# Kernel tuning notes

Hardware: AMD Instinct MI355X
Metric: run time of the kernel (lower is better)

## Reference

```python
import jax, jax.numpy as jnp
import numpy as np

NUM_HEADS = 16
D_MODEL = 1024
D_K = D_MODEL // NUM_HEADS
THETA = 10000.0
SEQ_LEN = 2048
BATCH = 2


def _rope(x, token_positions):
    # x: [B, H, S, d_k]; token_positions: [S] int
    d_k = x.shape[-1]
    inv_freq = THETA ** (-jnp.arange(0, d_k, 2, dtype=jnp.float32) / d_k)  # [d_k/2]
    ang = token_positions.astype(jnp.float32)[:, None] * inv_freq[None, :]  # [S, d_k/2]
    cos, sin = jnp.cos(ang), jnp.sin(ang)
    x_even = x[..., ::2]
    x_odd = x[..., 1::2]
    rot_even = x_even * cos - x_odd * sin
    rot_odd = x_even * sin + x_odd * cos
    return jnp.stack([rot_even, rot_odd], axis=-1).reshape(x.shape)


def setup_inputs() -> dict:
    key = jax.random.key(0)
    kx, kq, kk, kv, ko = jax.random.split(key, 5)
    sigma = float(np.sqrt(2.0 / (D_MODEL + D_MODEL)))
    x = jax.random.normal(kx, (BATCH, SEQ_LEN, D_MODEL), dtype=jnp.float32)
    Wq = jax.random.truncated_normal(kq, -3.0, 3.0, (D_MODEL, D_MODEL), jnp.float32) * sigma
    Wk = jax.random.truncated_normal(kk, -3.0, 3.0, (D_MODEL, D_MODEL), jnp.float32) * sigma
    Wv = jax.random.truncated_normal(kv, -3.0, 3.0, (D_MODEL, D_MODEL), jnp.float32) * sigma
    Wo = jax.random.truncated_normal(ko, -3.0, 3.0, (D_MODEL, D_MODEL), jnp.float32) * sigma
    token_positions = jnp.arange(SEQ_LEN, dtype=jnp.int32)
    return {"x": x, "Wq": Wq, "Wk": Wk, "Wv": Wv, "Wo": Wo, "token_positions": token_positions}


def reference(x, Wq, Wk, Wv, Wo, token_positions):
    bs, seq_len, _ = x.shape
    # Linear stores W as [out, in]: out = einsum('...i,oi->...o')
    def proj(W):
        h = jnp.einsum('bsi,oi->bso', x, W)
        return h.reshape(bs, seq_len, NUM_HEADS, D_K).transpose(0, 2, 1, 3)  # [B,H,S,d_k]
    Q = _rope(proj(Wq), token_positions)
    K = _rope(proj(Wk), token_positions)
    V = proj(Wv)
    scores = jnp.einsum('bhqd,bhkd->bhqk', Q, K) / jnp.sqrt(jnp.float32(D_K))
    causal = jnp.tril(jnp.ones((seq_len, seq_len), dtype=bool))
    scores = jnp.where(causal[None, None], scores, -jnp.inf)
    probs = jax.nn.softmax(scores, axis=-1)
    attn = jnp.einsum('bhqk,bhkd->bhqd', probs, V)
    attn = attn.transpose(0, 2, 1, 3).reshape(bs, seq_len, NUM_HEADS * D_K)
    return jnp.einsum('bsi,oi->bso', attn, Wo)
```

## Files before the change

kernel.cpp:

```cpp
#include <hip/hip_runtime.h>
#include <math.h>

#define SEQ  2048
#define DM   1024
#define NH   16
#define DK   64
#define MTOT 4096
#define BATCH 2

typedef __attribute__((ext_vector_type(8))) short bf16x8;
typedef __attribute__((ext_vector_type(4))) float f32x4;

#define CSC 0.18033688011112042f

__device__ __forceinline__ ushort f2bf(float f) {
    unsigned u = __builtin_bit_cast(unsigned, f);
    u += 0x7FFFu + ((u >> 16) & 1u);
    return (ushort)(u >> 16);
}

__device__ __forceinline__ void async_ld16(const void* g, void* l) {
    __builtin_amdgcn_global_load_lds(
        (const __attribute__((address_space(1))) void*)g,
        (__attribute__((address_space(3))) void*)l, 16, 0, 0);
}


__global__ __launch_bounds__(256) void convert_kernel(
    const float* __restrict__ X, const float* __restrict__ Wq,
    const float* __restrict__ Wk, const float* __restrict__ Wv,
    const float* __restrict__ Wo, const int* __restrict__ pos,
    ushort* __restrict__ Xb, ushort* __restrict__ Wqkvb,
    ushort* __restrict__ Wob, float2* __restrict__ rtab)
{
    const int y = blockIdx.y;
    if (y == 5) {
        int i = blockIdx.x * 256 + threadIdx.x;
        if (i < SEQ * 32) {
            int s = i >> 5, j = i & 31;
            float freq = exp2f(-(float)(2 * j) * (13.287712379549449f / 64.0f));
            float ang = (float)pos[s] * freq;
            float sn, cs;
            sincosf(ang, &sn, &cs);
            rtab[i] = make_float2(cs, sn);
        }
        return;
    }
    const float* src; ushort* dst; int n;
    if (y == 0)      { src = X;  dst = Xb;                 n = MTOT * DM; }
    else if (y == 1) { src = Wq; dst = Wqkvb;              n = DM * DM; }
    else if (y == 2) { src = Wk; dst = Wqkvb + DM * DM;    n = DM * DM; }
    else if (y == 3) { src = Wv; dst = Wqkvb + 2 * DM * DM; n = DM * DM; }
    else             { src = Wo; dst = Wob;                n = DM * DM; }
    for (int i = (blockIdx.x * 256 + threadIdx.x) * 4; i < n; i += gridDim.x * 256 * 4) {
        float4 v = *(const float4*)(src + i);
        ushort4 o = { f2bf(v.x), f2bf(v.y), f2bf(v.z), f2bf(v.w) };
        *(ushort4*)(dst + i) = o;
    }
}

template <int MODE>
__global__ __launch_bounds__(256, 3) void gemm_mfma(
    const ushort* __restrict__ Agl, const ushort* __restrict__ Bgl,
    const float2* __restrict__ rtab, ushort* __restrict__ O0,
    ushort* __restrict__ O1, ushort* __restrict__ O2,
    float* __restrict__ Fout)
{
    constexpr int BM = (MODE == 0) ? 128 : 64;
    constexpr int BN = 128;
    constexpr int BK = 32;
    constexpr int WM = (MODE == 0) ? 64 : 32;
    constexpr int MT = WM / 16;
    constexpr int NINST = (BM + BN) / 16;
    constexpr int PW = NINST / 4;

    __shared__ __align__(16) ushort S[(BM + BN) * BK];

    const int t    = threadIdx.x;
    const int lane = t & 63;
    const int w    = t >> 6;
    const int wm   = w >> 1, wn = w & 1;
    const int l16  = lane & 15, quad = lane >> 4;
    const int lrow = lane >> 2;
    const int lseg = (lane & 3) * 8;

    const int bn = blockIdx.x, bm = blockIdx.y;
    const int m0 = bm * BM, n0 = bn * BN;

    f32x4 acc[MT][4];
#pragma unroll
    for (int mt = 0; mt < MT; ++mt)
#pragma unroll
        for (int nt = 0; nt < 4; ++nt) acc[mt][nt] = (f32x4){0.f, 0.f, 0.f, 0.f};

    for (int kt = 0; kt < DM / BK; ++kt) {
        __syncthreads();
#pragma unroll
        for (int i = 0; i < PW; ++i) {
            const int rbase = (w * PW + i) * 16;
            const ushort* g;
            if (rbase < BM)
                g = Agl + (size_t)(m0 + rbase + lrow) * DM + kt * BK + lseg;
            else
                g = Bgl + (size_t)(n0 + rbase - BM + lrow) * DM + kt * BK + lseg;
            async_ld16(g, &S[rbase * BK]);
        }
        __syncthreads();

        bf16x8 af[MT], bfr[4];
#pragma unroll
        for (int mt = 0; mt < MT; ++mt)
            af[mt] = *(const bf16x8*)&S[(wm * WM + mt * 16 + l16) * BK + quad * 8];
#pragma unroll
        for (int nt = 0; nt < 4; ++nt)
            bfr[nt] = *(const bf16x8*)&S[(BM + wn * 64 + nt * 16 + l16) * BK + quad * 8];
#pragma unroll
        for (int mt = 0; mt < MT; ++mt)
#pragma unroll
            for (int nt = 0; nt < 4; ++nt)
                acc[mt][nt] = __builtin_amdgcn_mfma_f32_16x16x32_bf16(
                    af[mt], bfr[nt], acc[mt][nt], 0, 0, 0);
    }

    if (MODE == 1) {
#pragma unroll
        for (int mt = 0; mt < MT; ++mt)
#pragma unroll
            for (int r = 0; r < 4; ++r) {
                const int m = m0 + wm * WM + mt * 16 + quad * 4 + r;
#pragma unroll
                for (int nt = 0; nt < 4; ++nt) {
                    const int n = n0 + wn * 64 + nt * 16 + l16;
                    Fout[(size_t)m * DM + n] = acc[mt][nt][r];
                }
            }
    } else {
        const int matb = n0 >> 10;
        if (matb < 2) {
            ushort* img = matb ? O1 : O0;
            const int hh = ((n0 & 1023) + wn * 64) >> 6;
            int dloc[4];
#pragma unroll
            for (int nt = 0; nt < 4; ++nt) dloc[nt] = nt * 16 + l16;
#pragma unroll
            for (int mt = 0; mt < MT; ++mt)
#pragma unroll
                for (int r = 0; r < 4; ++r) {
                    const int m = m0 + wm * WM + mt * 16 + quad * 4 + r;
                    const int bb = m >> 11;
                    const int s = m & 2047;
                    const size_t base =
                        ((size_t)(bb * NH + hh) * 32 + (s >> 6)) * 4096 + (s & 63) * 64;
                    const int swz = s & 7;
#pragma unroll
                    for (int nt = 0; nt < 4; ++nt) {
                        const float v = acc[mt][nt][r];
                        const float vp = __shfl_xor(v, 1);
                        const float2 cs = rtab[s * 32 + (dloc[nt] >> 1)];
                        float res = (dloc[nt] & 1) ? (vp * cs.y + v * cs.x)
                                                   : (v * cs.x - vp * cs.y);
                        if (matb == 0) res *= CSC;
                        const int d = dloc[nt];
                        img[base + (((d >> 3) ^ swz) << 3) + (d & 7)] = f2bf(res);
                    }
                }
        } else {
#pragma unroll
            for (int mt = 0; mt < MT; ++mt)
#pragma unroll
                for (int r = 0; r < 4; ++r) {
                    const int m = m0 + wm * WM + mt * 16 + quad * 4 + r;
                    const int bb = m >> 11;
                    const int s = m & 2047;
#pragma unroll
                    for (int nt = 0; nt < 4; ++nt) {
                        const int dgl = (n0 & 1023) + wn * 64 + nt * 16 + l16;
                        const int hh = dgl >> 6, dd = dgl & 63;
                        const size_t off =
                            ((size_t)(bb * NH + hh) * 32 + (s >> 6)) * 4096 + dd * 64 +
                            ((((s & 63) >> 3) ^ (dd & 7)) << 3) + (s & 7);
                        O2[off] = f2bf(acc[mt][nt][r]);
                    }
                }
        }
    }
}

__global__ __launch_bounds__(256, 2) void attn_mfma(
    const ushort* __restrict__ Qimg, const ushort* __restrict__ Kimg,
    const ushort* __restrict__ Vimg, ushort* __restrict__ Ob)
{
    const int t    = threadIdx.x;
    const int lane = t & 63;
    const int w    = t >> 6;
    const int l16  = lane & 15;
    const int quad = lane >> 4;
    const int swz  = l16 & 7;

    const int id = blockIdx.x;
    const int h  = id & 15;
    const int z  = id >> 4;
    const int b  = z & 1;
    const int p  = z >> 1;
    const int qtB = 31 - p;

    const size_t bh = ((size_t)(b * NH + h)) * 32;
    const ushort* Kh = Kimg + bh * 4096;
    const ushort* Vh = Vimg + bh * 4096;

    __shared__ __align__(16) ushort Ks[2][4096];
    __shared__ __align__(16) ushort Vs[2][4096];
    __shared__ __align__(16) ushort Ps[4096];

#define STAGE_KV(tile, buf)                                                  \
    do {                                                                     \
        const ushort* Kt_ = Kh + (size_t)(tile) * 4096;                      \
        const ushort* Vt_ = Vh + (size_t)(tile) * 4096;                      \
        _Pragma("unroll") for (int i_ = 0; i_ < 2; ++i_) {                   \
            async_ld16(Kt_ + i_ * 2048 + w * 512 + lane * 8,                 \
                       &Ks[buf][i_ * 2048 + w * 512]);                       \
            async_ld16(Vt_ + i_ * 2048 + w * 512 + lane * 8,                 \
                       &Vs[buf][i_ * 2048 + w * 512]);                       \
        }                                                                    \
    } while (0)

    const int qr = w * 16 + l16;

    bf16x8 bQ0, bQ1;
    {
        const ushort* Qt = Qimg + (bh + p) * 4096;
        bQ0 = *(const bf16x8*)(Qt + qr * 64 + ((quad ^ swz) << 3));
        bQ1 = *(const bf16x8*)(Qt + qr * 64 + (((4 + quad) ^ swz) << 3));
    }

    STAGE_KV(0, 0);

    f32x4 Oacc[4];
    float m_i = -1e30f, l_i = 0.f;
#pragma unroll
    for (int d = 0; d < 4; ++d) Oacc[d] = (f32x4){0.f, 0.f, 0.f, 0.f};

    int qt = p;

    auto writeO = [&](int qtw) {
#pragma unroll
        for (int r = 0; r < 4; ++r) {
            const float lr = __shfl(l_i, (lane & 48) | (quad * 4 + r));
            const float inv = 1.0f / lr;
            const int q_abs = qtw * 64 + w * 16 + quad * 4 + r;
            ushort* dst = Ob + (size_t)(b * SEQ + q_abs) * DM + h * DK + l16;
#pragma unroll
            for (int dblk = 0; dblk < 4; ++dblk)
                dst[dblk * 16] = f2bf(Oacc[dblk][r] * inv);
        }
    };

    for (int it = 0; it <= 32; ++it) {
        const int cur = it & 1;
        const int kt = (it <= p) ? it : it - (p + 1);
        __syncthreads();

        if (it < 32) {
            const int itn = it + 1;
            const int ktn = (itn <= p) ? itn : itn - (p + 1);
            STAGE_KV(ktn, cur ^ 1);
        }

        bf16x8 aK[4][2];
#pragma unroll
        for (int ki = 0; ki < 4; ++ki)
#pragma unroll
            for (int ds = 0; ds < 2; ++ds)
                aK[ki][ds] = *(const bf16x8*)
                    &Ks[cur][(ki * 16 + l16) * 64 + (((ds * 4 + quad) ^ swz) << 3)];
        bf16x8 bV[2][4];
#pragma unroll
        for (int s2 = 0; s2 < 2; ++s2)
#pragma unroll
            for (int dblk = 0; dblk < 4; ++dblk)
                bV[s2][dblk] = *(const bf16x8*)
                    &Vs[cur][(dblk * 16 + l16) * 64 + (((s2 * 4 + quad) ^ swz) << 3)];

        f32x4 Sc[4];
#pragma unroll
        for (int ki = 0; ki < 4; ++ki) {
            Sc[ki] = (f32x4){0.f, 0.f, 0.f, 0.f};
            Sc[ki] = __builtin_amdgcn_mfma_f32_16x16x32_bf16(aK[ki][0], bQ0, Sc[ki], 0, 0, 0);
            Sc[ki] = __builtin_amdgcn_mfma_f32_16x16x32_bf16(aK[ki][1], bQ1, Sc[ki], 0, 0, 0);
        }

        float ts[4][4];
        float mloc = -1e30f;
        if (kt == qt) {
            const int qa = w * 16 + l16;
            const int ka = quad * 4;
#pragma unroll
            for (int ki = 0; ki < 4; ++ki)
#pragma unroll
                for (int r = 0; r < 4; ++r) {
                    float v = Sc[ki][r];
                    if (ka + ki * 16 + r > qa) v = -1e30f;
                    ts[ki][r] = v;
                    mloc = fmaxf(mloc, v);
                }
        } else {
#pragma unroll
            for (int ki = 0; ki < 4; ++ki)
#pragma unroll
                for (int r = 0; r < 4; ++r) {
                    ts[ki][r] = Sc[ki][r];
                    mloc = fmaxf(mloc, Sc[ki][r]);
                }
        }
        mloc = fmaxf(mloc, __shfl_xor(mloc, 16));
        mloc = fmaxf(mloc, __shfl_xor(mloc, 32));
        const float mnew = fmaxf(m_i, mloc);
        const float alpha = __builtin_amdgcn_exp2f(m_i - mnew);
        m_i = mnew;

        float psum = 0.f;
        const int prow = qr * 64;
        const int phalf = (quad & 1) * 4;
#pragma unroll
        for (int ki = 0; ki < 4; ++ki) {
            float p0 = __builtin_amdgcn_exp2f(ts[ki][0] - mnew);
            float p1 = __builtin_amdgcn_exp2f(ts[ki][1] - mnew);
            float p2 = __builtin_amdgcn_exp2f(ts[ki][2] - mnew);
            float p3 = __builtin_amdgcn_exp2f(ts[ki][3] - mnew);
            psum += (p0 + p1) + (p2 + p3);
            ushort4 pk = { f2bf(p0), f2bf(p1), f2bf(p2), f2bf(p3) };
            const int seg = ki * 2 + (quad >> 1);
            *(ushort4*)&Ps[prow + (((seg ^ swz) << 3) + phalf)] = pk;
        }
        psum += __shfl_xor(psum, 16);
        psum += __shfl_xor(psum, 32);
        l_i = l_i * alpha + psum;

        float ar[4];
#pragma unroll
        for (int r = 0; r < 4; ++r)
            ar[r] = __shfl(alpha, (lane & 48) | (quad * 4 + r));
#pragma unroll
        for (int dblk = 0; dblk < 4; ++dblk)
#pragma unroll
            for (int r = 0; r < 4; ++r) Oacc[dblk][r] *= ar[r];

#pragma unroll
        for (int s2 = 0; s2 < 2; ++s2) {
            bf16x8 aP = *(const bf16x8*)&Ps[prow + (((s2 * 4 + quad) ^ swz) << 3)];
#pragma unroll
            for (int dblk = 0; dblk < 4; ++dblk)
                Oacc[dblk] = __builtin_amdgcn_mfma_f32_16x16x32_bf16(
                    aP, bV[s2][dblk], Oacc[dblk], 0, 0, 0);
        }

        if (it == p) {
            writeO(p);
            m_i = -1e30f; l_i = 0.f;
#pragma unroll
            for (int d = 0; d < 4; ++d) Oacc[d] = (f32x4){0.f, 0.f, 0.f, 0.f};
            qt = qtB;
            const ushort* Qt = Qimg + (bh + qtB) * 4096;
            bQ0 = *(const bf16x8*)(Qt + qr * 64 + ((quad ^ swz) << 3));
            bQ1 = *(const bf16x8*)(Qt + qr * 64 + (((4 + quad) ^ swz) << 3));
        }
    }

    writeO(qtB);
#undef STAGE_KV
}

extern "C" void kernel_launch(void* const* d_in, const int* in_sizes, int n_in,
                              void* d_out, int out_size, void* d_ws, size_t ws_size,
                              hipStream_t stream)
{
    const float* x  = (const float*)d_in[0];
    const float* Wq = (const float*)d_in[1];
    const float* Wk = (const float*)d_in[2];
    const float* Wv = (const float*)d_in[3];
    const float* Wo = (const float*)d_in[4];
    const int* pos  = (const int*)d_in[5];
    float* out = (float*)d_out;

    ushort* Xb    = (ushort*)d_ws;
    ushort* Wqkvb = Xb + (size_t)MTOT * DM;
    ushort* Wob   = Wqkvb + (size_t)3 * DM * DM;
    float2* rtab  = (float2*)(Wob + (size_t)DM * DM);
    ushort* Qimg  = (ushort*)(rtab + SEQ * 32);
    ushort* Kimg  = Qimg + (size_t)MTOT * DM;
    ushort* Vimg  = Kimg + (size_t)MTOT * DM;
    ushort* attnb = Vimg + (size_t)MTOT * DM;

    dim3 blk(256);
    convert_kernel<<<dim3(1024, 6), blk, 0, stream>>>(
        x, Wq, Wk, Wv, Wo, pos, Xb, Wqkvb, Wob, rtab);
    gemm_mfma<0><<<dim3(24, 32), blk, 0, stream>>>(
        Xb, Wqkvb, rtab, Qimg, Kimg, Vimg, nullptr);
    attn_mfma<<<dim3(512), blk, 0, stream>>>(Qimg, Kimg, Vimg, attnb);
    gemm_mfma<1><<<dim3(8, 64), blk, 0, stream>>>(
        attnb, Wob, nullptr, nullptr, nullptr, nullptr, out);
}
```

Baseline: 187.5 us.

## Halve attention block to two waves, each handling two 16-row query fragments

The attention kernel now runs 128 threads per block instead of 256. Each wave processes 32 query rows as two 16-row fragments, so every K/V fragment read from LDS feeds twice as many MFMAs. The bf16 packing of P switches from round-to-nearest to truncation via a byte-permute, which is cheaper but slightly less accurate. In exchange there are fewer waves per block, so latency hiding drops and register pressure rises, and each thread issues more async staging loads.

```diff
diff --git a/kernel.cpp b/kernel.cpp
--- a/kernel.cpp
+++ b/kernel.cpp
@@ -186,7 +186,7 @@
     }
 }
 
-__global__ __launch_bounds__(256, 2) void attn_mfma(
+__global__ __launch_bounds__(128, 2) void attn_mfma(
     const ushort* __restrict__ Qimg, const ushort* __restrict__ Kimg,
     const ushort* __restrict__ Vimg, ushort* __restrict__ Ob)
 {
@@ -216,43 +216,49 @@
     do {                                                                     \
         const ushort* Kt_ = Kh + (size_t)(tile) * 4096;                      \
         const ushort* Vt_ = Vh + (size_t)(tile) * 4096;                      \
-        _Pragma("unroll") for (int i_ = 0; i_ < 2; ++i_) {                   \
-            async_ld16(Kt_ + i_ * 2048 + w * 512 + lane * 8,                 \
-                       &Ks[buf][i_ * 2048 + w * 512]);                       \
-            async_ld16(Vt_ + i_ * 2048 + w * 512 + lane * 8,                 \
-                       &Vs[buf][i_ * 2048 + w * 512]);                       \
+        _Pragma("unroll") for (int i_ = 0; i_ < 4; ++i_) {                   \
+            async_ld16(Kt_ + i_ * 1024 + t * 8, &Ks[buf][i_ * 1024 + t * 8]);\
+            async_ld16(Vt_ + i_ * 1024 + t * 8, &Vs[buf][i_ * 1024 + t * 8]);\
         }                                                                    \
     } while (0)
 
-    const int qr = w * 16 + l16;
-
-    bf16x8 bQ0, bQ1;
+    bf16x8 bQ[2][2];
     {
         const ushort* Qt = Qimg + (bh + p) * 4096;
-        bQ0 = *(const bf16x8*)(Qt + qr * 64 + ((quad ^ swz) << 3));
-        bQ1 = *(const bf16x8*)(Qt + qr * 64 + (((4 + quad) ^ swz) << 3));
+#pragma unroll
+        for (int f = 0; f < 2; ++f) {
+            const int row = w * 32 + f * 16 + l16;
+            bQ[f][0] = *(const bf16x8*)(Qt + row * 64 + ((quad ^ swz) << 3));
+            bQ[f][1] = *(const bf16x8*)(Qt + row * 64 + (((4 + quad) ^ swz) << 3));
+        }
     }
 
     STAGE_KV(0, 0);
 
-    f32x4 Oacc[4];
-    float m_i = -1e30f, l_i = 0.f;
-#pragma unroll
-    for (int d = 0; d < 4; ++d) Oacc[d] = (f32x4){0.f, 0.f, 0.f, 0.f};
+    f32x4 Oacc[2][4];
+    float m_i[2], l_i[2];
+#pragma unroll
+    for (int f = 0; f < 2; ++f) {
+        m_i[f] = -1e30f; l_i[f] = 0.f;
+#pragma unroll
+        for (int d = 0; d < 4; ++d) Oacc[f][d] = (f32x4){0.f, 0.f, 0.f, 0.f};
+    }
 
     int qt = p;
 
     auto writeO = [&](int qtw) {
 #pragma unroll
-        for (int r = 0; r < 4; ++r) {
-            const float lr = __shfl(l_i, (lane & 48) | (quad * 4 + r));
-            const float inv = 1.0f / lr;
-            const int q_abs = qtw * 64 + w * 16 + quad * 4 + r;
-            ushort* dst = Ob + (size_t)(b * SEQ + q_abs) * DM + h * DK + l16;
-#pragma unroll
-            for (int dblk = 0; dblk < 4; ++dblk)
-                dst[dblk * 16] = f2bf(Oacc[dblk][r] * inv);
-        }
+        for (int f = 0; f < 2; ++f)
+#pragma unroll
+            for (int r = 0; r < 4; ++r) {
+                const float lr = __shfl(l_i[f], (lane & 48) | (quad * 4 + r));
+                const float inv = 1.0f / lr;
+                const int q_abs = qtw * 64 + w * 32 + f * 16 + quad * 4 + r;
+                ushort* dst = Ob + (size_t)(b * SEQ + q_abs) * DM + h * DK + l16;
+#pragma unroll
+                for (int dblk = 0; dblk < 4; ++dblk)
+                    dst[dblk * 16] = f2bf(Oacc[f][dblk][r] * inv);
+            }
     };
 
     for (int it = 0; it <= 32; ++it) {
@@ -281,88 +287,104 @@
                 bV[s2][dblk] = *(const bf16x8*)
                     &Vs[cur][(dblk * 16 + l16) * 64 + (((s2 * 4 + quad) ^ swz) << 3)];
 
-        f32x4 Sc[4];
-#pragma unroll
-        for (int ki = 0; ki < 4; ++ki) {
-            Sc[ki] = (f32x4){0.f, 0.f, 0.f, 0.f};
-            Sc[ki] = __builtin_amdgcn_mfma_f32_16x16x32_bf16(aK[ki][0], bQ0, Sc[ki], 0, 0, 0);
-            Sc[ki] = __builtin_amdgcn_mfma_f32_16x16x32_bf16(aK[ki][1], bQ1, Sc[ki], 0, 0, 0);
-        }
-
-        float ts[4][4];
-        float mloc = -1e30f;
-        if (kt == qt) {
-            const int qa = w * 16 + l16;
-            const int ka = quad * 4;
-#pragma unroll
-            for (int ki = 0; ki < 4; ++ki)
-#pragma unroll
-                for (int r = 0; r < 4; ++r) {
-                    float v = Sc[ki][r];
-                    if (ka + ki * 16 + r > qa) v = -1e30f;
-                    ts[ki][r] = v;
-                    mloc = fmaxf(mloc, v);
-                }
-        } else {
-#pragma unroll
-            for (int ki = 0; ki < 4; ++ki)
-#pragma unroll
-                for (int r = 0; r < 4; ++r) {
-                    ts[ki][r] = Sc[ki][r];
-                    mloc = fmaxf(mloc, Sc[ki][r]);
-                }
-        }
-        mloc = fmaxf(mloc, __shfl_xor(mloc, 16));
-        mloc = fmaxf(mloc, __shfl_xor(mloc, 32));
-        const float mnew = fmaxf(m_i, mloc);
-        const float alpha = __builtin_amdgcn_exp2f(m_i - mnew);
-        m_i = mnew;
-
-        float psum = 0.f;
-        const int prow = qr * 64;
-        const int phalf = (quad & 1) * 4;
-#pragma unroll
-        for (int ki = 0; ki < 4; ++ki) {
-            float p0 = __builtin_amdgcn_exp2f(ts[ki][0] - mnew);
-            float p1 = __builtin_amdgcn_exp2f(ts[ki][1] - mnew);
-            float p2 = __builtin_amdgcn_exp2f(ts[ki][2] - mnew);
-            float p3 = __builtin_amdgcn_exp2f(ts[ki][3] - mnew);
-            psum += (p0 + p1) + (p2 + p3);
-            ushort4 pk = { f2bf(p0), f2bf(p1), f2bf(p2), f2bf(p3) };
-            const int seg = ki * 2 + (quad >> 1);
-            *(ushort4*)&Ps[prow + (((seg ^ swz) << 3) + phalf)] = pk;
-        }
-        psum += __shfl_xor(psum, 16);
-        psum += __shfl_xor(psum, 32);
-        l_i = l_i * alpha + psum;
-
-        float ar[4];
-#pragma unroll
-        for (int r = 0; r < 4; ++r)
-            ar[r] = __shfl(alpha, (lane & 48) | (quad * 4 + r));
-#pragma unroll
-        for (int dblk = 0; dblk < 4; ++dblk)
-#pragma unroll
-            for (int r = 0; r < 4; ++r) Oacc[dblk][r] *= ar[r];
-
-#pragma unroll
-        for (int s2 = 0; s2 < 2; ++s2) {
-            bf16x8 aP = *(const bf16x8*)&Ps[prow + (((s2 * 4 + quad) ^ swz) << 3)];
+#pragma unroll
+        for (int f = 0; f < 2; ++f) {
+            f32x4 Sc[4];
+#pragma unroll
+            for (int ki = 0; ki < 4; ++ki) {
+                Sc[ki] = (f32x4){0.f, 0.f, 0.f, 0.f};
+                Sc[ki] = __builtin_amdgcn_mfma_f32_16x16x32_bf16(aK[ki][0], bQ[f][0], Sc[ki], 0, 0, 0);
+                Sc[ki] = __builtin_amdgcn_mfma_f32_16x16x32_bf16(aK[ki][1], bQ[f][1], Sc[ki], 0, 0, 0);
+            }
+
+            float ts[4][4];
+            float mloc = -1e30f;
+            if (kt == qt) {
+                const int qa = w * 32 + f * 16 + l16;
+                const int ka = quad * 4;
+#pragma unroll
+                for (int ki = 0; ki < 4; ++ki)
+#pragma unroll
+                    for (int r = 0; r < 4; ++r) {
+                        float v = Sc[ki][r];
+                        if (ka + ki * 16 + r > qa) v = -1e30f;
+                        ts[ki][r] = v;
+                        mloc = fmaxf(mloc, v);
+                    }
+            } else {
+#pragma unroll
+                for (int ki = 0; ki < 4; ++ki)
+#pragma unroll
+                    for (int r = 0; r < 4; ++r) {
+                        ts[ki][r] = Sc[ki][r];
+                        mloc = fmaxf(mloc, Sc[ki][r]);
+                    }
+            }
+            mloc = fmaxf(mloc, __shfl_xor(mloc, 16));
+            mloc = fmaxf(mloc, __shfl_xor(mloc, 32));
+            const float mnew = fmaxf(m_i[f], mloc);
+            const float alpha = __builtin_amdgcn_exp2f(m_i[f] - mnew);
+            m_i[f] = mnew;
+
+            float psum = 0.f;
+            const int prow = (w * 32 + f * 16 + l16) * 64;
+            const int phalf = (quad & 1) * 4;
+#pragma unroll
+            for (int ki = 0; ki < 4; ++ki) {
+                float p0 = __builtin_amdgcn_exp2f(ts[ki][0] - mnew);
+                float p1 = __builtin_amdgcn_exp2f(ts[ki][1] - mnew);
+                float p2 = __builtin_amdgcn_exp2f(ts[ki][2] - mnew);
+                float p3 = __builtin_amdgcn_exp2f(ts[ki][3] - mnew);
+                psum += (p0 + p1) + (p2 + p3);
+                uint2 pk;
+                pk.x = __builtin_amdgcn_perm(__builtin_bit_cast(unsigned, p1),
+                                             __builtin_bit_cast(unsigned, p0),
+                                             0x07060302u);
+                pk.y = __builtin_amdgcn_perm(__builtin_bit_cast(unsigned, p3),
+                                             __builtin_bit_cast(unsigned, p2),
+                                             0x07060302u);
+                const int seg = ki * 2 + (quad >> 1);
+                *(uint2*)&Ps[prow + (((seg ^ swz) << 3) + phalf)] = pk;
+            }
+            psum += __shfl_xor(psum, 16);
+            psum += __shfl_xor(psum, 32);
+            l_i[f] = l_i[f] * alpha + psum;
+
+            float ar[4];
+#pragma unroll
+            for (int r = 0; r < 4; ++r)
+                ar[r] = __shfl(alpha, (lane & 48) | (quad * 4 + r));
 #pragma unroll
             for (int dblk = 0; dblk < 4; ++dblk)
-                Oacc[dblk] = __builtin_amdgcn_mfma_f32_16x16x32_bf16(
-                    aP, bV[s2][dblk], Oacc[dblk], 0, 0, 0);
+#pragma unroll
+                for (int r = 0; r < 4; ++r) Oacc[f][dblk][r] *= ar[r];
+
+#pragma unroll
+            for (int s2 = 0; s2 < 2; ++s2) {
+                bf16x8 aP = *(const bf16x8*)&Ps[prow + (((s2 * 4 + quad) ^ swz) << 3)];
+#pragma unroll
+                for (int dblk = 0; dblk < 4; ++dblk)
+                    Oacc[f][dblk] = __builtin_amdgcn_mfma_f32_16x16x32_bf16(
+                        aP, bV[s2][dblk], Oacc[f][dblk], 0, 0, 0);
+            }
         }
 
         if (it == p) {
             writeO(p);
-            m_i = -1e30f; l_i = 0.f;
-#pragma unroll
-            for (int d = 0; d < 4; ++d) Oacc[d] = (f32x4){0.f, 0.f, 0.f, 0.f};
+#pragma unroll
+            for (int f = 0; f < 2; ++f) {
+                m_i[f] = -1e30f; l_i[f] = 0.f;
+#pragma unroll
+                for (int d = 0; d < 4; ++d) Oacc[f][d] = (f32x4){0.f, 0.f, 0.f, 0.f};
+            }
             qt = qtB;
             const ushort* Qt = Qimg + (bh + qtB) * 4096;
-            bQ0 = *(const bf16x8*)(Qt + qr * 64 + ((quad ^ swz) << 3));
-            bQ1 = *(const bf16x8*)(Qt + qr * 64 + (((4 + quad) ^ swz) << 3));
+#pragma unroll
+            for (int f = 0; f < 2; ++f) {
+                const int row = w * 32 + f * 16 + l16;
+                bQ[f][0] = *(const bf16x8*)(Qt + row * 64 + ((quad ^ swz) << 3));
+                bQ[f][1] = *(const bf16x8*)(Qt + row * 64 + (((4 + quad) ^ swz) << 3));
+            }
         }
     }
 
@@ -391,12 +413,11 @@
     ushort* Vimg  = Kimg + (size_t)MTOT * DM;
     ushort* attnb = Vimg + (size_t)MTOT * DM;
 
-    dim3 blk(256);
-    convert_kernel<<<dim3(1024, 6), blk, 0, stream>>>(
+    convert_kernel<<<dim3(1024, 6), dim3(256), 0, stream>>>(
         x, Wq, Wk, Wv, Wo, pos, Xb, Wqkvb, Wob, rtab);
-    gemm_mfma<0><<<dim3(24, 32), blk, 0, stream>>>(
+    gemm_mfma<0><<<dim3(24, 32), dim3(256), 0, stream>>>(
         Xb, Wqkvb, rtab, Qimg, Kimg, Vimg, nullptr);
-    attn_mfma<<<dim3(512), blk, 0, stream>>>(Qimg, Kimg, Vimg, attnb);
-    gemm_mfma<1><<<dim3(8, 64), blk, 0, stream>>>(
+    attn_mfma<<<dim3(512), dim3(128), 0, stream>>>(Qimg, Kimg, Vimg, attnb);
+    gemm_mfma<1><<<dim3(8, 64), dim3(256), 0, stream>>>(
         attnb, Wob, nullptr, nullptr, nullptr, nullptr, out);
 }
```

Result: slower. 196.8 us (+5.0%).
